# Performance work log

Hardware: AMD Instinct MI355X
Metric: run time of the kernel (lower is better)

Reference implementation:

```python
import jax, jax.numpy as jnp
import numpy as np

H = 12      # num_attention_heads
DH = 64     # attention_head_size
D = H * DH  # hidden_size = 768
EPS = 1e-12

def setup_inputs() -> dict:
    key = jax.random.key(0)
    ks = jax.random.split(key, 12)
    B, S = 8, 1024
    s = 0.02
    return {
        "hidden_states": jax.random.normal(ks[0], (B, S, D), jnp.float32),
        "attention_mask": jnp.zeros((B, 1, 1, S), jnp.float32),
        "Wq": jax.random.normal(ks[1], (D, D), jnp.float32) * s,
        "bq": jnp.zeros((D,), jnp.float32),
        "Wk": jax.random.normal(ks[2], (D, D), jnp.float32) * s,
        "bk": jnp.zeros((D,), jnp.float32),
        "Wv": jax.random.normal(ks[3], (D, D), jnp.float32) * s,
        "bv": jnp.zeros((D,), jnp.float32),
        "Wd": jax.random.normal(ks[4], (D, D), jnp.float32) * s,
        "bd": jnp.zeros((D,), jnp.float32),
        "ln_g": jnp.ones((D,), jnp.float32),
        "ln_b": jnp.zeros((D,), jnp.float32),
    }

def _heads(x, W, b):
    # [B,S,D] -> [B,H,S,Dh]
    B, S, _ = x.shape
    y = x @ W.T + b
    return y.reshape(B, S, H, DH).transpose(0, 2, 1, 3)

def reference(hidden_states, attention_mask, Wq, bq, Wk, bk, Wv, bv, Wd, bd, ln_g, ln_b):
    q = _heads(hidden_states, Wq, bq)
    k = _heads(hidden_states, Wk, bk)
    v = _heads(hidden_states, Wv, bv)
    scores = jnp.einsum('bhqd,bhkd->bhqk', q, k) / np.sqrt(DH).astype(np.float32)
    scores = scores + attention_mask  # broadcast [B,1,1,S]
    probs = jax.nn.softmax(scores, axis=-1)
    ctx = jnp.einsum('bhqk,bhkd->bhqd', probs, v)
    B, _, S, _ = ctx.shape
    ctx = ctx.transpose(0, 2, 1, 3).reshape(B, S, D)
    out = ctx @ Wd.T + bd  # dropout = identity (eval)
    x = hidden_states + out
    mu = jnp.mean(x, axis=-1, keepdims=True)
    var = jnp.var(x, axis=-1, keepdims=True)
    return (x - mu) / jnp.sqrt(var + EPS) * ln_g + ln_b
```

## Files before the change

### kernel.cpp

```cpp
#include <hip/hip_runtime.h>

typedef unsigned short u16;
typedef unsigned int u32;

#define H_ 12
#define DH_ 64
#define D_ 768
#define S_ 1024
#define B_ 8
#define M_TOT 8192
#define LOG2E 1.44269504089f

using f32x4  = __attribute__((ext_vector_type(4))) float;
using bf16x8 = __attribute__((ext_vector_type(8))) short;

__device__ inline u16 f2bf(float f) {
  union { float f; u32 u; } v; v.f = f;
  u32 r = v.u + 0x7FFFu + ((v.u >> 16) & 1u);
  return (u16)(r >> 16);
}

__device__ inline void gload_lds16(const u16* g, u16* l) {
  __builtin_amdgcn_global_load_lds((const __attribute__((address_space(1))) void*)g,
                                   (__attribute__((address_space(3))) void*)l, 16, 0, 0);
}

__global__ void convert_all(const float* __restrict__ X,
                            const float* __restrict__ Wq, const float* __restrict__ Wk,
                            const float* __restrict__ Wv, const float* __restrict__ Wd,
                            u16* __restrict__ Xb, u16* __restrict__ Wqkv, u16* __restrict__ Wdb) {
  int stride = gridDim.x * blockDim.x;
  int tid = blockIdx.x * blockDim.x + threadIdx.x;
  const int NX4 = M_TOT * D_ / 4;
  const int NW4 = D_ * D_ / 4;
  const int NW = D_ * D_;
  for (int i = tid; i < NX4; i += stride) {
    float4 x = ((const float4*)X)[i];
    uint2 p;
    p.x = (u32)f2bf(x.x) | ((u32)f2bf(x.y) << 16);
    p.y = (u32)f2bf(x.z) | ((u32)f2bf(x.w) << 16);
    ((uint2*)Xb)[i] = p;
  }
  for (int i = tid; i < NW4; i += stride) {
    float4 q = ((const float4*)Wq)[i];
    float4 k = ((const float4*)Wk)[i];
    float4 v = ((const float4*)Wv)[i];
    float4 d = ((const float4*)Wd)[i];
    uint2 pq, pk, pv, pd;
    pq.x = (u32)f2bf(q.x) | ((u32)f2bf(q.y) << 16); pq.y = (u32)f2bf(q.z) | ((u32)f2bf(q.w) << 16);
    pk.x = (u32)f2bf(k.x) | ((u32)f2bf(k.y) << 16); pk.y = (u32)f2bf(k.z) | ((u32)f2bf(k.w) << 16);
    pv.x = (u32)f2bf(v.x) | ((u32)f2bf(v.y) << 16); pv.y = (u32)f2bf(v.z) | ((u32)f2bf(v.w) << 16);
    pd.x = (u32)f2bf(d.x) | ((u32)f2bf(d.y) << 16); pd.y = (u32)f2bf(d.z) | ((u32)f2bf(d.w) << 16);
    ((uint2*)Wqkv)[i]            = pq;
    ((uint2*)(Wqkv + NW))[i]     = pk;
    ((uint2*)(Wqkv + 2*NW))[i]   = pv;
    ((uint2*)Wdb)[i]             = pd;
  }
}

#define NT_ 24

__global__ __launch_bounds__(256, 4) void gemm_qkv(
    const u16* __restrict__ A, const u16* __restrict__ Bw,
    const float* __restrict__ bq, const float* __restrict__ bk, const float* __restrict__ bv,
    u16* __restrict__ Q, u16* __restrict__ K, u16* __restrict__ Vt) {
  __shared__ u16 As[2 * 128 * 32];
  __shared__ u16 Bs[2 * 128 * 32];
  int tid = threadIdx.x, lane = tid & 63, wave = tid >> 6;
  int wg = blockIdx.x;
  int xcd = wg & 7, li = wg >> 3;
  int m0 = (xcd * 8 + (li & 7)) * 128;
  int n0 = (li >> 3) * 128;
  int wm = (wave >> 1) * 64, wn = (wave & 1) * 64;
  int fr = lane & 15, fg = lane >> 4;
  f32x4 acc[4][4] = {};

  int srow = tid >> 2;
  int schunk = (lane & 3) ^ ((lane >> 3) & 3);
  const u16* AgS = A  + (size_t)(m0 + srow) * D_ + schunk * 8;
  const u16* BgS = Bw + (size_t)(n0 + srow) * D_ + schunk * 8;
  u16* Abase = &As[wave * 512];
  u16* Bbase = &Bs[wave * 512];
  int ra = (fg ^ ((fr >> 1) & 3)) * 8;

  gload_lds16(AgS,            Abase);
  gload_lds16(AgS + 64 * D_,  Abase + 2048);
  gload_lds16(BgS,            Bbase);
  gload_lds16(BgS + 64 * D_,  Bbase + 2048);
  __syncthreads();

  for (int t = 0; t < NT_; ++t) {
    int cur = t & 1, nxt = cur ^ 1;
    if (t < NT_ - 1) {
      int k1 = (t + 1) * 32;
      gload_lds16(AgS + k1,           Abase + nxt * 4096);
      gload_lds16(AgS + 64 * D_ + k1, Abase + nxt * 4096 + 2048);
      gload_lds16(BgS + k1,           Bbase + nxt * 4096);
      gload_lds16(BgS + 64 * D_ + k1, Bbase + nxt * 4096 + 2048);
    }
    bf16x8 af[4], bf[4];
#pragma unroll
    for (int i = 0; i < 4; i++) {
      af[i] = *(const bf16x8*)&As[cur * 4096 + (wm + i * 16 + fr) * 32 + ra];
      bf[i] = *(const bf16x8*)&Bs[cur * 4096 + (wn + i * 16 + fr) * 32 + ra];
    }
    __builtin_amdgcn_s_setprio(1);
#pragma unroll
    for (int mi = 0; mi < 4; mi++)
#pragma unroll
      for (int ni = 0; ni < 4; ni++)
        acc[mi][ni] = __builtin_amdgcn_mfma_f32_16x16x32_bf16(af[mi], bf[ni], acc[mi][ni], 0, 0, 0);
    __builtin_amdgcn_s_setprio(0);
    __syncthreads();
  }

  int which = n0 / D_;
  int ncol0 = n0 % D_;
  const float* bias = (which == 0) ? bq : (which == 1) ? bk : bv;
  if (which == 2) {
#pragma unroll
    for (int mi = 0; mi < 4; mi++)
#pragma unroll
      for (int ni = 0; ni < 4; ni++) {
        int col = ncol0 + wn + ni*16 + fr;
        float bb = bias[col];
        int row = m0 + wm + mi*16 + fg*4;
        int bidx = row >> 10, s = row & 1023;
        int hh = col >> 6, dd = col & 63;
        u16 t0 = f2bf(acc[mi][ni][0] + bb);
        u16 t1 = f2bf(acc[mi][ni][1] + bb);
        u16 t2 = f2bf(acc[mi][ni][2] + bb);
        u16 t3 = f2bf(acc[mi][ni][3] + bb);
        uint2 pk2;
        pk2.x = (u32)t0 | ((u32)t1 << 16);
        pk2.y = (u32)t2 | ((u32)t3 << 16);
        *(uint2*)(Vt + ((size_t)((bidx * H_ + hh) * DH_ + dd)) * S_ + s) = pk2;
      }
  } else {
    u16* Out = (which == 0) ? Q : K;
    float scale = (which == 0) ? (0.125f * LOG2E) : 1.0f;
#pragma unroll
    for (int mi = 0; mi < 4; mi++)
#pragma unroll
      for (int ni = 0; ni < 4; ni++) {
        int col = ncol0 + wn + ni*16 + fr;
        float bb = bias[col];
#pragma unroll
        for (int r = 0; r < 4; r++) {
          int row = m0 + wm + mi*16 + fg*4 + r;
          Out[row * D_ + col] = f2bf((acc[mi][ni][r] + bb) * scale);
        }
      }
  }
}

__global__ __launch_bounds__(256, 4) void gemm_out(
    const u16* __restrict__ A, const u16* __restrict__ Bw,
    const float* __restrict__ bd, const float* __restrict__ hidden,
    float* __restrict__ Tmp) {
  __shared__ u16 As[2 * 64 * 32];
  __shared__ u16 Bs[2 * 128 * 32];
  int tid = threadIdx.x, lane = tid & 63, wave = tid >> 6;
  int wg = blockIdx.x;
  int xcd = wg & 7, li = wg >> 3;
  int m0 = (xcd * 16 + (li & 15)) * 64;
  int n0 = (li >> 4) * 128;
  int wm = (wave >> 1) * 32, wn = (wave & 1) * 64;
  int fr = lane & 15, fg = lane >> 4;
  f32x4 acc[2][4] = {};

  int srow = tid >> 2;
  int schunk = (lane & 3) ^ ((lane >> 3) & 3);
  const u16* AgS = A  + (size_t)(m0 + srow) * D_ + schunk * 8;
  const u16* BgS = Bw + (size_t)(n0 + srow) * D_ + schunk * 8;
  u16* Abase = &As[wave * 512];
  u16* Bbase = &Bs[wave * 512];
  int ra = (fg ^ ((fr >> 1) & 3)) * 8;

  gload_lds16(AgS,            Abase);
  gload_lds16(BgS,            Bbase);
  gload_lds16(BgS + 64 * D_,  Bbase + 2048);
  __syncthreads();

  for (int t = 0; t < NT_; ++t) {
    int cur = t & 1, nxt = cur ^ 1;
    if (t < NT_ - 1) {
      int k1 = (t + 1) * 32;
      gload_lds16(AgS + k1,           Abase + nxt * 2048);
      gload_lds16(BgS + k1,           Bbase + nxt * 4096);
      gload_lds16(BgS + 64 * D_ + k1, Bbase + nxt * 4096 + 2048);
    }
    bf16x8 af[2], bf[4];
#pragma unroll
    for (int i = 0; i < 2; i++)
      af[i] = *(const bf16x8*)&As[cur * 2048 + (wm + i * 16 + fr) * 32 + ra];
#pragma unroll
    for (int i = 0; i < 4; i++)
      bf[i] = *(const bf16x8*)&Bs[cur * 4096 + (wn + i * 16 + fr) * 32 + ra];
    __builtin_amdgcn_s_setprio(1);
#pragma unroll
    for (int mi = 0; mi < 2; mi++)
#pragma unroll
      for (int ni = 0; ni < 4; ni++)
        acc[mi][ni] = __builtin_amdgcn_mfma_f32_16x16x32_bf16(af[mi], bf[ni], acc[mi][ni], 0, 0, 0);
    __builtin_amdgcn_s_setprio(0);
    __syncthreads();
  }

#pragma unroll
  for (int mi = 0; mi < 2; mi++)
#pragma unroll
    for (int ni = 0; ni < 4; ni++) {
      int col = n0 + wn + ni*16 + fr;
      float bb = bd[col];
#pragma unroll
      for (int r = 0; r < 4; r++) {
        int row = m0 + wm + mi*16 + fg*4 + r;
        Tmp[row * D_ + col] = acc[mi][ni][r] + bb + hidden[row * D_ + col];
      }
    }
}

#define KB 64
#define LDK 72
#define QW 32

__global__ __launch_bounds__(256) void attn_kernel(
    const u16* __restrict__ Q, const u16* __restrict__ K, const u16* __restrict__ Vt,
    const float* __restrict__ mask, u16* __restrict__ Ctx) {
  __shared__ u16 Ks[KB * LDK];
  __shared__ u16 Vs[DH_ * LDK];
  __shared__ u16 Ps[4 * QW * LDK];
  __shared__ float Ms[S_];
  int tid = threadIdx.x, lane = tid & 63, wave = tid >> 6;
  int i = blockIdx.x;
  int xcd = i & 7, slot = i >> 3;
  int bh = xcd * 12 + (slot >> 3);
  int qt = slot & 7;
  int b = bh / H_, h = bh % H_;
  int q0 = qt * 128 + wave * QW;
  int fr = lane & 15, fg = lane >> 4;

  {
    float4 m4 = ((const float4*)(mask + b * S_))[tid];
    m4.x *= LOG2E; m4.y *= LOG2E; m4.z *= LOG2E; m4.w *= LOG2E;
    ((float4*)Ms)[tid] = m4;
  }

  bf16x8 qf[2][2];
#pragma unroll
  for (int s = 0; s < 2; s++) {
    const u16* Qrow = Q + (size_t)(b * S_ + q0 + s*16 + fr) * D_ + h * DH_;
    qf[s][0] = *(const bf16x8*)(Qrow + fg * 8);
    qf[s][1] = *(const bf16x8*)(Qrow + 32 + fg * 8);
  }

  f32x4 acc[2][4] = {};
  float l_part[2] = {0.f, 0.f};

  int srow = tid >> 2;
  int scc = (tid & 3) * 16;
  const u16* Kg0 = K  + (size_t)(b * S_ + srow) * D_ + h * DH_ + scc;
  const u16* Vg0 = Vt + (size_t)(bh * DH_ + srow) * S_ + scc;
  u16* Pw = &Ps[wave * QW * LDK];

  for (int kt = 0; kt < S_; kt += KB) {
    __syncthreads();
    {
      const u16* Kg = Kg0 + (size_t)kt * D_;
      const u16* Vg = Vg0 + kt;
      *(int4*)&Ks[srow * LDK + scc]     = *(const int4*)Kg;
      *(int4*)&Ks[srow * LDK + scc + 8] = *(const int4*)(Kg + 8);
      *(int4*)&Vs[srow * LDK + scc]     = *(const int4*)Vg;
      *(int4*)&Vs[srow * LDK + scc + 8] = *(const int4*)(Vg + 8);
    }
    __syncthreads();

    f32x4 mv[4];
#pragma unroll
    for (int kb = 0; kb < 4; kb++) {
      float4 t = *(const float4*)&Ms[kt + kb*16 + fg*4];
      mv[kb][0] = t.x; mv[kb][1] = t.y; mv[kb][2] = t.z; mv[kb][3] = t.w;
    }

#pragma unroll
    for (int s = 0; s < 2; s++) {
#pragma unroll
      for (int kb = 0; kb < 4; kb++) {
        bf16x8 kf0 = *(const bf16x8*)&Ks[(kb*16 + fr) * LDK + fg*8];
        bf16x8 kf1 = *(const bf16x8*)&Ks[(kb*16 + fr) * LDK + 32 + fg*8];
        f32x4 sv = mv[kb];
        sv = __builtin_amdgcn_mfma_f32_16x16x32_bf16(kf0, qf[s][0], sv, 0, 0, 0);
        sv = __builtin_amdgcn_mfma_f32_16x16x32_bf16(kf1, qf[s][1], sv, 0, 0, 0);
        float p0 = __builtin_amdgcn_exp2f(sv[0]);
        float p1 = __builtin_amdgcn_exp2f(sv[1]);
        float p2 = __builtin_amdgcn_exp2f(sv[2]);
        float p3 = __builtin_amdgcn_exp2f(sv[3]);
        l_part[s] += (p0 + p1) + (p2 + p3);
        u32 lo, hi;
        asm("v_cvt_pk_bf16_f32 %0, %1, %2" : "=v"(lo) : "v"(p0), "v"(p1));
        asm("v_cvt_pk_bf16_f32 %0, %1, %2" : "=v"(hi) : "v"(p2), "v"(p3));
        uint2 pk2; pk2.x = lo; pk2.y = hi;
        *(uint2*)&Pw[(s*16 + fr) * LDK + kb*16 + fg*4] = pk2;
      }
    }

    bf16x8 pf[2][2];
#pragma unroll
    for (int s = 0; s < 2; s++) {
      pf[s][0] = *(const bf16x8*)&Pw[(s*16 + fr) * LDK + fg*8];
      pf[s][1] = *(const bf16x8*)&Pw[(s*16 + fr) * LDK + 32 + fg*8];
    }
    __builtin_amdgcn_s_setprio(1);
#pragma unroll
    for (int ns = 0; ns < 4; ns++) {
      bf16x8 vf0 = *(const bf16x8*)&Vs[(ns*16 + fr) * LDK + fg*8];
      bf16x8 vf1 = *(const bf16x8*)&Vs[(ns*16 + fr) * LDK + 32 + fg*8];
#pragma unroll
      for (int s = 0; s < 2; s++) {
        acc[s][ns] = __builtin_amdgcn_mfma_f32_16x16x32_bf16(pf[s][0], vf0, acc[s][ns], 0, 0, 0);
        acc[s][ns] = __builtin_amdgcn_mfma_f32_16x16x32_bf16(pf[s][1], vf1, acc[s][ns], 0, 0, 0);
      }
    }
    __builtin_amdgcn_s_setprio(0);
  }

  float li[2][4];
#pragma unroll
  for (int s = 0; s < 2; s++) {
    l_part[s] += __shfl_xor(l_part[s], 16);
    l_part[s] += __shfl_xor(l_part[s], 32);
    float inv = 1.0f / l_part[s];
#pragma unroll
    for (int r = 0; r < 4; r++)
      li[s][r] = __shfl(inv, fg*4 + r);
  }
#pragma unroll
  for (int s = 0; s < 2; s++) {
    u16* Crow = Ctx + (size_t)(b * S_ + q0 + s*16) * D_ + h * DH_;
#pragma unroll
    for (int ns = 0; ns < 4; ns++)
#pragma unroll
      for (int r = 0; r < 4; r++)
        Crow[(fg*4 + r) * D_ + ns*16 + fr] = f2bf(acc[s][ns][r] * li[s][r]);
  }
}

__global__ __launch_bounds__(256) void ln_kernel(
    const float* __restrict__ Tmp, const float* __restrict__ g,
    const float* __restrict__ bta, float* __restrict__ out) {
  int wave = threadIdx.x >> 6, lane = threadIdx.x & 63;
  int row = blockIdx.x * 4 + wave;
  const float4* x4 = (const float4*)(Tmp + (size_t)row * D_);
  const float4* g4 = (const float4*)g;
  const float4* b4 = (const float4*)bta;
  float4* o4 = (float4*)(out + (size_t)row * D_);
  float4 v[3];
  float s = 0.f, s2 = 0.f;
#pragma unroll
  for (int w = 0; w < 3; w++) {
    v[w] = x4[lane + w * 64];
    s  += v[w].x + v[w].y + v[w].z + v[w].w;
    s2 += v[w].x*v[w].x + v[w].y*v[w].y + v[w].z*v[w].z + v[w].w*v[w].w;
  }
#pragma unroll
  for (int m = 1; m < 64; m <<= 1) { s += __shfl_xor(s, m); s2 += __shfl_xor(s2, m); }
  float mean = s * (1.0f / D_);
  float var = s2 * (1.0f / D_) - mean * mean;
  float inv = rsqrtf(var + 1e-12f);
#pragma unroll
  for (int w = 0; w < 3; w++) {
    float4 gg = g4[lane + w * 64];
    float4 bb = b4[lane + w * 64];
    float4 o;
    o.x = (v[w].x - mean) * inv * gg.x + bb.x;
    o.y = (v[w].y - mean) * inv * gg.y + bb.y;
    o.z = (v[w].z - mean) * inv * gg.z + bb.z;
    o.w = (v[w].w - mean) * inv * gg.w + bb.w;
    o4[lane + w * 64] = o;
  }
}

extern "C" void kernel_launch(void* const* d_in, const int* in_sizes, int n_in,
                              void* d_out, int out_size, void* d_ws, size_t ws_size,
                              hipStream_t stream) {
  (void)in_sizes; (void)n_in; (void)out_size; (void)ws_size;
  const float* hidden = (const float*)d_in[0];
  const float* mask   = (const float*)d_in[1];
  const float* Wq = (const float*)d_in[2];
  const float* bq = (const float*)d_in[3];
  const float* Wk = (const float*)d_in[4];
  const float* bk = (const float*)d_in[5];
  const float* Wv = (const float*)d_in[6];
  const float* bv = (const float*)d_in[7];
  const float* Wd = (const float*)d_in[8];
  const float* bd = (const float*)d_in[9];
  const float* ln_g = (const float*)d_in[10];
  const float* ln_b = (const float*)d_in[11];
  float* out = (float*)d_out;

  char* ws = (char*)d_ws;
  u16* Xb    = (u16*)(ws);
  u16* Wqkv  = (u16*)(ws + 12582912);
  u16* Wdb   = (u16*)(ws + 16121856);
  u16* Q     = (u16*)(ws + 17301504);
  u16* K     = (u16*)(ws + 29884416);
  u16* Vt    = (u16*)(ws + 42467328);
  u16* Ctx   = (u16*)(ws + 55050240);
  float* Tmp = (float*)(ws + 17301504);

  convert_all<<<2048, 256, 0, stream>>>(hidden, Wq, Wk, Wv, Wd, Xb, Wqkv, Wdb);
  gemm_qkv<<<1152, 256, 0, stream>>>(Xb, Wqkv, bq, bk, bv, Q, K, Vt);
  attn_kernel<<<768, 256, 0, stream>>>(Q, K, Vt, mask, Ctx);
  gemm_out<<<768, 256, 0, stream>>>(Ctx, Wdb, bd, hidden, Tmp);
  ln_kernel<<<2048, 256, 0, stream>>>(Tmp, ln_g, ln_b, out);
}
```

Before: 132.7 us.

## Double-buffer K/V tiles with register prefetch and XOR-swizzled LDS layout

The attention kernel now prefetches the next K and V tile from global memory into registers while the current tile is being computed, then writes it into a second LDS buffer. This leaves one barrier per iteration instead of two. The padded LDS rows are replaced by an XOR swizzle to avoid bank conflicts, and the per-wave P buffer shrinks to a single 16-row slice that is reused for each query sub-block. This costs more registers and double the K/V LDS, which may reduce occupancy.

```diff
diff --git a/kernel.cpp b/kernel.cpp
--- a/kernel.cpp
+++ b/kernel.cpp
@@ -221,16 +221,12 @@
     }
 }
 
-#define KB 64
-#define LDK 72
-#define QW 32
-
 __global__ __launch_bounds__(256) void attn_kernel(
     const u16* __restrict__ Q, const u16* __restrict__ K, const u16* __restrict__ Vt,
     const float* __restrict__ mask, u16* __restrict__ Ctx) {
-  __shared__ u16 Ks[KB * LDK];
-  __shared__ u16 Vs[DH_ * LDK];
-  __shared__ u16 Ps[4 * QW * LDK];
+  __shared__ u16 Ks[2][64 * 64];
+  __shared__ u16 Vs[2][64 * 64];
+  __shared__ u16 Ps[4][16 * 64];
   __shared__ float Ms[S_];
   int tid = threadIdx.x, lane = tid & 63, wave = tid >> 6;
   int i = blockIdx.x;
@@ -238,7 +234,7 @@
   int bh = xcd * 12 + (slot >> 3);
   int qt = slot & 7;
   int b = bh / H_, h = bh % H_;
-  int q0 = qt * 128 + wave * QW;
+  int q0 = qt * 128 + wave * 32;
   int fr = lane & 15, fg = lane >> 4;
 
   {
@@ -255,43 +251,67 @@
     qf[s][1] = *(const bf16x8*)(Qrow + 32 + fg * 8);
   }
 
+  int srow = tid >> 2;
+  int scc = (tid & 3) * 16;
+  int sw = (srow & 7) << 3;
+  int sidx0 = srow * 64 + (scc ^ sw);
+  int sidx1 = srow * 64 + ((scc + 8) ^ sw);
+  const u16* Kg0 = K  + (size_t)(b * S_ + srow) * D_ + h * DH_ + scc;
+  const u16* Vg0 = Vt + (size_t)(bh * DH_ + srow) * S_ + scc;
+
+  int frw = (fr & 7) << 3;
+  int rc0 = (fg * 8) ^ frw;
+  int rc1 = (32 + fg * 8) ^ frw;
+  int pcw[4];
+#pragma unroll
+  for (int kb = 0; kb < 4; kb++) pcw[kb] = (kb * 16 + fg * 4) ^ frw;
+
   f32x4 acc[2][4] = {};
   float l_part[2] = {0.f, 0.f};
 
-  int srow = tid >> 2;
-  int scc = (tid & 3) * 16;
-  const u16* Kg0 = K  + (size_t)(b * S_ + srow) * D_ + h * DH_ + scc;
-  const u16* Vg0 = Vt + (size_t)(bh * DH_ + srow) * S_ + scc;
-  u16* Pw = &Ps[wave * QW * LDK];
-
-  for (int kt = 0; kt < S_; kt += KB) {
-    __syncthreads();
-    {
-      const u16* Kg = Kg0 + (size_t)kt * D_;
-      const u16* Vg = Vg0 + kt;
-      *(int4*)&Ks[srow * LDK + scc]     = *(const int4*)Kg;
-      *(int4*)&Ks[srow * LDK + scc + 8] = *(const int4*)(Kg + 8);
-      *(int4*)&Vs[srow * LDK + scc]     = *(const int4*)Vg;
-      *(int4*)&Vs[srow * LDK + scc + 8] = *(const int4*)(Vg + 8);
-    }
-    __syncthreads();
+  int4 kr0 = *(const int4*)Kg0;
+  int4 kr1 = *(const int4*)(Kg0 + 8);
+  int4 vr0 = *(const int4*)Vg0;
+  int4 vr1 = *(const int4*)(Vg0 + 8);
+  *(int4*)&Ks[0][sidx0] = kr0; *(int4*)&Ks[0][sidx1] = kr1;
+  *(int4*)&Vs[0][sidx0] = vr0; *(int4*)&Vs[0][sidx1] = vr1;
+  __syncthreads();
+
+  u16* Pw = Ps[wave];
+
+  for (int t = 0; t < 16; ++t) {
+    int cur = t & 1;
+    int kt = t * 64;
+    if (t < 15) {
+      const u16* Kg = Kg0 + (size_t)(kt + 64) * D_;
+      const u16* Vg = Vg0 + (kt + 64);
+      kr0 = *(const int4*)Kg; kr1 = *(const int4*)(Kg + 8);
+      vr0 = *(const int4*)Vg; vr1 = *(const int4*)(Vg + 8);
+    }
 
     f32x4 mv[4];
 #pragma unroll
     for (int kb = 0; kb < 4; kb++) {
-      float4 t = *(const float4*)&Ms[kt + kb*16 + fg*4];
-      mv[kb][0] = t.x; mv[kb][1] = t.y; mv[kb][2] = t.z; mv[kb][3] = t.w;
-    }
-
+      float4 m4 = *(const float4*)&Ms[kt + kb*16 + fg*4];
+      mv[kb][0] = m4.x; mv[kb][1] = m4.y; mv[kb][2] = m4.z; mv[kb][3] = m4.w;
+    }
+
+    bf16x8 kf[4][2];
+#pragma unroll
+    for (int kb = 0; kb < 4; kb++) {
+      int r = kb * 16 + fr;
+      kf[kb][0] = *(const bf16x8*)&Ks[cur][r * 64 + rc0];
+      kf[kb][1] = *(const bf16x8*)&Ks[cur][r * 64 + rc1];
+    }
+
+    bf16x8 pf[2][2];
 #pragma unroll
     for (int s = 0; s < 2; s++) {
 #pragma unroll
       for (int kb = 0; kb < 4; kb++) {
-        bf16x8 kf0 = *(const bf16x8*)&Ks[(kb*16 + fr) * LDK + fg*8];
-        bf16x8 kf1 = *(const bf16x8*)&Ks[(kb*16 + fr) * LDK + 32 + fg*8];
         f32x4 sv = mv[kb];
-        sv = __builtin_amdgcn_mfma_f32_16x16x32_bf16(kf0, qf[s][0], sv, 0, 0, 0);
-        sv = __builtin_amdgcn_mfma_f32_16x16x32_bf16(kf1, qf[s][1], sv, 0, 0, 0);
+        sv = __builtin_amdgcn_mfma_f32_16x16x32_bf16(kf[kb][0], qf[s][0], sv, 0, 0, 0);
+        sv = __builtin_amdgcn_mfma_f32_16x16x32_bf16(kf[kb][1], qf[s][1], sv, 0, 0, 0);
         float p0 = __builtin_amdgcn_exp2f(sv[0]);
         float p1 = __builtin_amdgcn_exp2f(sv[1]);
         float p2 = __builtin_amdgcn_exp2f(sv[2]);
@@ -301,21 +321,18 @@
         asm("v_cvt_pk_bf16_f32 %0, %1, %2" : "=v"(lo) : "v"(p0), "v"(p1));
         asm("v_cvt_pk_bf16_f32 %0, %1, %2" : "=v"(hi) : "v"(p2), "v"(p3));
         uint2 pk2; pk2.x = lo; pk2.y = hi;
-        *(uint2*)&Pw[(s*16 + fr) * LDK + kb*16 + fg*4] = pk2;
+        *(uint2*)&Pw[fr * 64 + pcw[kb]] = pk2;
       }
-    }
-
-    bf16x8 pf[2][2];
-#pragma unroll
-    for (int s = 0; s < 2; s++) {
-      pf[s][0] = *(const bf16x8*)&Pw[(s*16 + fr) * LDK + fg*8];
-      pf[s][1] = *(const bf16x8*)&Pw[(s*16 + fr) * LDK + 32 + fg*8];
-    }
+      pf[s][0] = *(const bf16x8*)&Pw[fr * 64 + rc0];
+      pf[s][1] = *(const bf16x8*)&Pw[fr * 64 + rc1];
+    }
+
     __builtin_amdgcn_s_setprio(1);
 #pragma unroll
     for (int ns = 0; ns < 4; ns++) {
-      bf16x8 vf0 = *(const bf16x8*)&Vs[(ns*16 + fr) * LDK + fg*8];
-      bf16x8 vf1 = *(const bf16x8*)&Vs[(ns*16 + fr) * LDK + 32 + fg*8];
+      int r = ns * 16 + fr;
+      bf16x8 vf0 = *(const bf16x8*)&Vs[cur][r * 64 + rc0];
+      bf16x8 vf1 = *(const bf16x8*)&Vs[cur][r * 64 + rc1];
 #pragma unroll
       for (int s = 0; s < 2; s++) {
         acc[s][ns] = __builtin_amdgcn_mfma_f32_16x16x32_bf16(pf[s][0], vf0, acc[s][ns], 0, 0, 0);
@@ -323,6 +340,13 @@
       }
     }
     __builtin_amdgcn_s_setprio(0);
+
+    if (t < 15) {
+      int nxt = cur ^ 1;
+      *(int4*)&Ks[nxt][sidx0] = kr0; *(int4*)&Ks[nxt][sidx1] = kr1;
+      *(int4*)&Vs[nxt][sidx0] = vr0; *(int4*)&Vs[nxt][sidx1] = vr1;
+      __syncthreads();
+    }
   }
 
   float li[2][4];
```

Measured after the change: 124.1 us. -6.5%, faster.
